# Optimization experiments

Hardware: AMD Instinct MI355X
Metric: run time of the kernel (lower is better)

## Reference

```python
import jax, jax.numpy as jnp
import numpy as np

B, K, N, T, C = 2, 2, 4096, 8, 3
H = 192            # hidden_dim
NODE_DIM = 10
N_LAYERS = 10
KNN = 16           # k nearest neighbours
TOP_FRAC = 0.4
SHARP = 5.0        # mask_sharpness
S = max(int(TOP_FRAC * N), KNN + 1)   # n_select per graph


def _ln(x, g, b, eps=1e-5):
    mu = x.mean(-1, keepdims=True)
    v = ((x - mu) ** 2).mean(-1, keepdims=True)  # biased var, matches nn.LayerNorm
    return (x - mu) / jnp.sqrt(v + eps) * g + b


def setup_inputs() -> dict:
    key = jax.random.key(0)
    ks = jax.random.split(key, 12)
    rn = lambda k, shape: 0.05 * jax.random.normal(k, shape, jnp.float32)
    F0 = 2 * NODE_DIM + 4   # first EdgeConv MLP in-dim
    FR = 2 * H + 4          # remaining EdgeConv MLP in-dim
    L = N_LAYERS - 1
    return {
        "u_base": jax.random.normal(ks[0], (B, K, N, C), jnp.float32),
        "pos": jax.random.uniform(ks[1], (B, N, 3), dtype=jnp.float32),
        "velocity_in": jax.random.normal(ks[2], (B, T, N, C), jnp.float32),
        "airfoil_mask": (jax.random.uniform(ks[3], (B, N)) < 0.05).astype(jnp.float32),
        "conv0_w1": rn(ks[4], (F0, H)), "conv0_b1": jnp.zeros((H,)),
        "conv0_w2": rn(ks[5], (H, H)), "conv0_b2": jnp.zeros((H,)),
        "conv0_g": jnp.ones((H,)), "conv0_be": jnp.zeros((H,)),
        "convs_w1": rn(ks[6], (L, FR, H)), "convs_b1": jnp.zeros((L, H)),
        "convs_w2": rn(ks[7], (L, H, H)), "convs_b2": jnp.zeros((L, H)),
        "convs_g": jnp.ones((L, H)), "convs_be": jnp.zeros((L, H)),
        "head_g": jnp.ones((H,)), "head_be": jnp.zeros((H,)),
        "head_w1": rn(ks[8], (H, H)), "head_b1": jnp.zeros((H,)),
        "head_w2": rn(ks[9], (H, 3)), "head_b2": jnp.zeros((3,)),
    }


def reference(u_base, pos, velocity_in, airfoil_mask,
              conv0_w1, conv0_b1, conv0_w2, conv0_b2, conv0_g, conv0_be,
              convs_w1, convs_b1, convs_w2, convs_b2, convs_g, convs_be,
              head_g, head_be, head_w1, head_b1, head_w2, head_b2):
    # --- variance gating (torch .var/.std are unbiased) ---
    var_pp = jnp.var(velocity_in, axis=1, ddof=1).sum(-1)                      # [B,N]
    var_z = (var_pp - var_pp.mean(1, keepdims=True)) / (
        jnp.std(var_pp, axis=1, ddof=1, keepdims=True) + 1e-8)
    soft_mask = jax.nn.sigmoid(SHARP * var_z) * (1.0 - airfoil_mask)           # [B,N]

    # --- select top-variance points per graph ---
    _, top_idx = jax.lax.top_k(var_pp, S)                                      # [B,S]
    pos_sel = jnp.take_along_axis(pos, top_idx[..., None], axis=1)             # [B,S,3]
    mask_sel = jnp.take_along_axis(soft_mask, top_idx, axis=1)[..., None]      # [B,S,1]
    v_last = velocity_in[:, -1]                                                # [B,N,C]
    ub_sel = jnp.take_along_axis(u_base, top_idx[:, None, :, None], axis=2)    # [B,K,S,C]
    vl_sel = jnp.take_along_axis(v_last, top_idx[..., None], axis=1)           # [B,S,C]
    vf_sel = jnp.take_along_axis(var_pp[..., None], top_idx[..., None], axis=1)
    static = jnp.concatenate([vl_sel, pos_sel, vf_sel], -1)                    # [B,S,7]
    x0 = jnp.concatenate(
        [ub_sel, jnp.broadcast_to(static[:, None], (B, K, S, 7))], -1)         # [B,K,S,10]

    def per_graph(x, pos_b):  # x: [K,S,F0], pos_b: [S,3]
        # kNN graph (self excluded via +inf diagonal, as in the chunked cdist)
        d2 = jnp.sum((pos_b[:, None] - pos_b[None]) ** 2, -1)                  # [S,S]
        d2 = d2.at[jnp.arange(S), jnp.arange(S)].set(jnp.inf)
        _, knn = jax.lax.top_k(-d2, KNN)                                       # [S,KNN]
        # PyG convention with edge_index=stack([targets, sources]):
        # i = edge_index[1] = knn neighbours, j = edge_index[0] = centre nodes
        idx_i = knn.reshape(-1)                     # [E] aggregation targets
        idx_j = jnp.repeat(jnp.arange(S), KNN)      # [E]
        rel = pos_b[idx_i] - pos_b[idx_j]           # pos[edge_index[1]] - pos[edge_index[0]]
        dist = jnp.linalg.norm(rel, axis=-1, keepdims=True)
        ea = jnp.concatenate([rel, dist], -1)       # [E,4]
        ea_b = jnp.broadcast_to(ea, (K,) + ea.shape)

        def conv(h, w1, b1, w2, b2, g, be):
            hi = h[:, idx_i]
            hj = h[:, idx_j]
            m = jnp.concatenate([hi, hj - hi, ea_b], -1)                       # [K,E,2F+4]
            m = jax.nn.gelu(m @ w1 + b1, approximate=False) @ w2 + b2          # [K,E,H]
            agg = jnp.zeros((K, S, H), h.dtype).at[:, idx_i].add(m)
            return _ln(agg, g, be)

        h = conv(x, conv0_w1, conv0_b1, conv0_w2, conv0_b2, conv0_g, conv0_be)
        for l in range(N_LAYERS - 1):
            h = conv(h, convs_w1[l], convs_b1[l], convs_w2[l], convs_b2[l],
                     convs_g[l], convs_be[l]) + h
        hh = _ln(h, head_g, head_be)
        return jax.nn.gelu(hh @ head_w1 + head_b1, approximate=False) @ head_w2 + head_b2

    delta = jax.vmap(per_graph)(x0, pos_sel)        # [B,K,S,3]
    delta = delta * mask_sel[:, None]               # [B,1,S,1]

    def scatter_b(idx, d):  # idx [S], d [K,S,3]
        return jnp.zeros((K, N, C), d.dtype).at[:, idx].set(d)

    delta_full = jax.vmap(scatter_b)(top_idx, delta)            # [B,K,N,C]
    return (u_base + delta_full) * (1.0 - airfoil_mask)[:, None, :, None]
```

## Files before the change

### kernel.cpp

```cpp
#include <hip/hip_runtime.h>
#include <hip/hip_bf16.h>
#include <math.h>

#define B_ 2
#define K_ 2
#define NN_ 4096
#define T_ 8
#define C_ 3
#define H_ 192
#define S_ 1638
#define KK_ 16
#define E_ (S_*KK_)
#define NROW (B_*K_*S_)
#define SHARP_ 5.0f

typedef __hip_bfloat16 bf;
typedef unsigned long long ull;
typedef __bf16 bf16x8 __attribute__((ext_vector_type(8)));
typedef float f32x4 __attribute__((ext_vector_type(4)));

__device__ int   g_isbf16;
__device__ __align__(16) float g_var[B_*NN_];
__device__ __align__(16) float g_vs1[B_*16];
__device__ __align__(16) float g_vs2[B_*16];
__device__ __align__(16) int   g_topidx[B_*S_];
__device__ __align__(16) float g_possel[B_*S_*3];
__device__ __align__(16) float g_masksel[B_*S_];
__device__ __align__(16) float g_x0[NROW*10];
__device__ __align__(16) int   g_knn[B_*E_];
__device__ __align__(16) float g_ea[B_*E_*4];
__device__ __align__(16) int   g_indeg[B_*S_];
__device__ __align__(16) int   g_cursor[B_*S_];
__device__ __align__(16) int   g_off[B_*(S_+1)];
__device__ __align__(16) int   g_list[B_*E_];
__device__ __align__(16) float g_P[(size_t)NROW*H_];
__device__ __align__(16) bf    g_Qbf[(size_t)NROW*H_];
__device__ __align__(16) float g_h[(size_t)NROW*H_];
__device__ __align__(16) bf    g_abf[(size_t)NROW*H_];
__device__ __align__(16) bf    g_w2p[(size_t)11*H_*H_];
__device__ __align__(16) bf    g_wcp[(size_t)9*H_*384];

__device__ __forceinline__ float bf2f(bf x){ return __bfloat162float(x); }
__device__ __forceinline__ float LD(const void* p, long i){
  return g_isbf16 ? __bfloat162float(((const bf*)p)[i]) : ((const float*)p)[i];
}
__device__ __forceinline__ float LDi(const void* p, long i, int isb){
  return isb ? __bfloat162float(((const bf*)p)[i]) : ((const float*)p)[i];
}
__device__ __forceinline__ float gelu_f(float x){ return 0.5f*x*(1.0f + erff(x*0.70710678118654752f)); }
__device__ __forceinline__ ull shfl_xor_u64(ull v, int m){
  unsigned lo = (unsigned)v, hi = (unsigned)(v >> 32);
  lo = __shfl_xor(lo, m, 64); hi = __shfl_xor(hi, m, 64);
  return ((ull)hi << 32) | lo;
}

__global__ __launch_bounds__(256) void k_var(const void* __restrict__ vel,
                                             const void* __restrict__ ub,
                                             const void* __restrict__ pos){
  __shared__ int s_bad;
  int b = blockIdx.y;
  int bx = blockIdx.x;
  int tid = threadIdx.x;
  if (tid == 0) s_bad = 0;
  __syncthreads();
  {
    const bf* pa = (const bf*)ub; const bf* pb = (const bf*)pos; const bf* pc = (const bf*)vel;
    int bad = 0;
    #pragma unroll
    for (int s = 0; s < 2; ++s){
      float va = __bfloat162float(pa[tid + s*256]);
      float vb = __bfloat162float(pb[tid + s*256]);
      float vc = __bfloat162float(pc[tid + s*256]);
      if (!(fabsf(va) <= 1000.f)) bad = 1;
      if (!(fabsf(vb) <= 1000.f)) bad = 1;
      if (!(fabsf(vc) <= 1000.f)) bad = 1;
    }
    if (bad) atomicOr(&s_bad, 1);
  }
  __syncthreads();
  int isb = (s_bad == 0) ? 1 : 0;
  if (bx == 0 && b == 0 && tid == 0) g_isbf16 = isb;
  int zi = (b*16 + bx)*256 + tid;
  if (zi < B_*S_){ g_indeg[zi] = 0; g_cursor[zi] = 0; }
  int n = bx*256 + tid;
  float v = 0.f;
  #pragma unroll
  for (int c = 0; c < 3; ++c){
    float x[8];
    #pragma unroll
    for (int t = 0; t < 8; ++t)
      x[t] = LDi(vel, ((long)(b*T_+t)*NN_ + n)*3 + c, isb);
    float m = __fadd_rn(__fadd_rn(__fadd_rn(x[0],x[1]), __fadd_rn(x[2],x[3])),
                        __fadd_rn(__fadd_rn(x[4],x[5]), __fadd_rn(x[6],x[7]))) / 8.0f;
    float d[8];
    #pragma unroll
    for (int t = 0; t < 8; ++t){ float dd = __fadd_rn(x[t], -m); d[t] = __fmul_rn(dd,dd); }
    float sv = __fadd_rn(__fadd_rn(__fadd_rn(d[0],d[1]), __fadd_rn(d[2],d[3])),
                         __fadd_rn(__fadd_rn(d[4],d[5]), __fadd_rn(d[6],d[7])));
    v = __fadd_rn(v, sv / 7.0f);
  }
  g_var[b*NN_ + n] = v;
  float s1 = v, s2 = v*v;
  #pragma unroll
  for (int o = 32; o; o >>= 1){ s1 += __shfl_xor(s1,o,64); s2 += __shfl_xor(s2,o,64); }
  __shared__ float r1[4], r2[4];
  int lane = tid & 63, wid = tid >> 6;
  if (!lane){ r1[wid]=s1; r2[wid]=s2; }
  __syncthreads();
  if (tid == 0){
    g_vs1[b*16 + bx] = r1[0]+r1[1]+r1[2]+r1[3];
    g_vs2[b*16 + bx] = r2[0]+r2[1]+r2[2]+r2[3];
  }
}

__global__ __launch_bounds__(256) void k_rank(){
  int b = blockIdx.y;
  int i = blockIdx.x*4 + (threadIdx.x >> 6);
  int lane = threadIdx.x & 63;
  float vi = g_var[b*NN_+i];
  int rank = 0;
  for (int j = lane; j < NN_; j += 64){
    float vj = g_var[b*NN_+j];
    rank += ((vj > vi) || (vj == vi && j < i)) ? 1 : 0;
  }
  #pragma unroll
  for (int o = 32; o; o >>= 1) rank += __shfl_xor(rank, o, 64);
  if (lane == 0 && rank < S_) g_topidx[b*S_ + rank] = i;
}

__global__ void k_gather(const void* __restrict__ pos, const void* __restrict__ ub,
                         const void* __restrict__ vel, const void* __restrict__ air){
  int gi = blockIdx.x*256 + threadIdx.x;
  if (gi >= B_*S_) return;
  int b = gi / S_, s = gi - b*S_;
  int node = g_topidx[gi];
  float px = LD(pos, ((long)b*NN_+node)*3+0);
  float py = LD(pos, ((long)b*NN_+node)*3+1);
  float pz = LD(pos, ((long)b*NN_+node)*3+2);
  g_possel[gi*3+0]=px; g_possel[gi*3+1]=py; g_possel[gi*3+2]=pz;
  float S1 = 0.f, S2 = 0.f;
  #pragma unroll
  for (int t = 0; t < 16; ++t){ S1 += g_vs1[b*16+t]; S2 += g_vs2[b*16+t]; }
  float mean = S1*(1.f/NN_);
  float sd = sqrtf(fmaxf((S2 - S1*S1*(1.f/NN_))*(1.f/(NN_-1)), 0.f));
  float vf = g_var[b*NN_+node];
  float z = (vf-mean)/(sd+1e-8f);
  float sig = 1.f/(1.f+expf(-SHARP_*z));
  g_masksel[gi] = sig*(1.f - LD(air, b*NN_+node));
  float vl0 = LD(vel, ((long)(b*T_+7)*NN_+node)*3+0);
  float vl1 = LD(vel, ((long)(b*T_+7)*NN_+node)*3+1);
  float vl2 = LD(vel, ((long)(b*T_+7)*NN_+node)*3+2);
  for (int k = 0; k < K_; ++k){
    long row = (long)(b*K_+k)*S_ + s;
    float* x = g_x0 + row*10;
    x[0]=LD(ub, ((long)(b*K_+k)*NN_+node)*3+0);
    x[1]=LD(ub, ((long)(b*K_+k)*NN_+node)*3+1);
    x[2]=LD(ub, ((long)(b*K_+k)*NN_+node)*3+2);
    x[3]=vl0; x[4]=vl1; x[5]=vl2;
    x[6]=px;  x[7]=py;  x[8]=pz;
    x[9]=vf;
  }
}

__global__ __launch_bounds__(256) void k_knn(){
  __shared__ float px[S_], py[S_], pz[S_];
  int b = blockIdx.y;
  int j = blockIdx.x*4 + (threadIdx.x >> 6);
  int lane = threadIdx.x & 63;
  for (int t = threadIdx.x; t < S_; t += 256){
    px[t] = g_possel[(b*S_+t)*3+0];
    py[t] = g_possel[(b*S_+t)*3+1];
    pz[t] = g_possel[(b*S_+t)*3+2];
  }
  __syncthreads();
  if (j >= S_) return;
  float xj=px[j], yj=py[j], zj=pz[j];
  float dist[KK_]; int id[KK_];
  #pragma unroll
  for (int t = 0; t < KK_; ++t){ dist[t]=3.0e38f; id[t]=0x7fffffff; }
  for (int c = lane; c < S_; c += 64){
    if (c == j) continue;
    float dx=__fadd_rn(px[c],-xj), dy=__fadd_rn(py[c],-yj), dz=__fadd_rn(pz[c],-zj);
    float d2 = __fadd_rn(__fadd_rn(__fmul_rn(dx,dx), __fmul_rn(dy,dy)), __fmul_rn(dz,dz));
    if (d2 < dist[KK_-1]){
      int p = 0;
      #pragma unroll
      for (int q = 0; q < KK_; ++q) p += (dist[q] <= d2) ? 1 : 0;
      #pragma unroll
      for (int q = KK_-1; q >= 1; --q){
        bool mv = (q > p);
        dist[q] = mv ? dist[q-1] : dist[q];
        id[q]   = mv ? id[q-1]   : id[q];
      }
      #pragma unroll
      for (int q = 0; q < KK_; ++q){ if (q == p){ dist[q] = d2; id[q] = c; } }
    }
  }
  ull mykey = 0;
  #pragma unroll
  for (int t = 0; t < KK_; ++t){
    ull k = (((ull)__float_as_uint(dist[0])) << 32) | (unsigned)id[0];
    ull m = k;
    #pragma unroll
    for (int o = 32; o; o >>= 1){ ull other = shfl_xor_u64(m, o); m = (other < m) ? other : m; }
    if (k == m){
      #pragma unroll
      for (int q = 0; q < KK_-1; ++q){ dist[q]=dist[q+1]; id[q]=id[q+1]; }
      dist[KK_-1] = 3.0e38f; id[KK_-1] = 0x7fffffff;
    }
    if (lane == t) mykey = m;
  }
  if (lane < KK_){
    int i = (int)(mykey & 0xffffffffu);
    g_knn[(b*S_+j)*KK_ + lane] = i;
    float rx = __fadd_rn(px[i],-xj), ry = __fadd_rn(py[i],-yj), rz = __fadd_rn(pz[i],-zj);
    float dd = sqrtf(__fadd_rn(__fadd_rn(__fmul_rn(rx,rx), __fmul_rn(ry,ry)), __fmul_rn(rz,rz)));
    float* o = g_ea + ((long)b*E_ + j*KK_ + lane)*4;
    o[0]=rx; o[1]=ry; o[2]=rz; o[3]=dd;
    atomicAdd(&g_indeg[b*S_+i], 1);
  }
}

__global__ void k_scan(){
  __shared__ int sA[2048], sB[2048];
  int b = blockIdx.x, tid = threadIdx.x;
  for (int i = tid; i < 2048; i += 1024) sA[i] = (i < S_) ? g_indeg[b*S_+i] : 0;
  __syncthreads();
  int *src = sA, *dst = sB;
  for (int d = 1; d < 2048; d <<= 1){
    for (int i = tid; i < 2048; i += 1024) dst[i] = src[i] + (i >= d ? src[i-d] : 0);
    __syncthreads();
    int* t2 = src; src = dst; dst = t2;
  }
  if (tid == 0) g_off[b*(S_+1)] = 0;
  for (int i = tid; i < S_; i += 1024) g_off[b*(S_+1)+i+1] = src[i];
}

#define PW2_BLKS 1584
#define PWC_BLKS 2592
#define INIT_BLKS 192
#define FILL_BLKS 205
#define PROJ_BLKS 410
__global__ void k_packall(const void* __restrict__ c0w2, const void* __restrict__ cw2,
                          const void* __restrict__ hw1, const void* __restrict__ cw1,
                          const void* __restrict__ ub, const void* __restrict__ air,
                          float* __restrict__ out, const void* __restrict__ c0w1){
  int blk = blockIdx.x;
  if (blk < PW2_BLKS){
    int gi = blk*256 + threadIdx.x;
    if (gi >= 11*H_*H_) return;
    int mat = gi / (H_*H_), r = gi - mat*(H_*H_);
    int k = r / H_, n = r - (r/H_)*H_;
    float v;
    if (mat == 0)      v = LD(c0w2, (long)k*H_ + n);
    else if (mat <= 9) v = LD(cw2, (long)(mat-1)*H_*H_ + (long)k*H_ + n);
    else               v = LD(hw1, (long)k*H_ + n);
    int t = k>>5, q = (k>>3)&3, jj = k&7;
    g_w2p[(size_t)mat*H_*H_ + (((t*4+q)*H_ + n)*8 + jj)] = __float2bfloat16(v);
  } else if (blk < PW2_BLKS + PWC_BLKS){
    int gi = (blk - PW2_BLKS)*256 + threadIdx.x;
    if (gi >= 9*H_*384) return;
    int l = gi / (H_*384), r = gi - l*(H_*384);
    int k = r / 384, n = r - (r/384)*384;
    long base = (long)l*388*H_;
    float v;
    if (n < H_) v = LD(cw1, base + (long)k*H_ + n) - LD(cw1, base + (long)(H_+k)*H_ + n);
    else        v = LD(cw1, base + (long)(H_+k)*H_ + (n-H_));
    int t = k>>5, q = (k>>3)&3, jj = k&7;
    g_wcp[(size_t)l*(H_*384) + (((t*4+q)*384 + n)*8 + jj)] = __float2bfloat16(v);
  } else if (blk < PW2_BLKS + PWC_BLKS + INIT_BLKS){
    int gi = (blk - PW2_BLKS - PWC_BLKS)*256 + threadIdx.x;
    int n = (gi/3) % NN_;
    int b = gi / (K_*NN_*C_);
    float a = 1.f - LD(air, b*NN_+n);
    out[gi] = LD(ub, gi) * a;
  } else if (blk < PW2_BLKS + PWC_BLKS + INIT_BLKS + FILL_BLKS){
    int idx = (blk - PW2_BLKS - PWC_BLKS - INIT_BLKS)*256 + threadIdx.x;
    if (idx >= B_*E_) return;
    int b = idx / E_, e = idx - b*E_;
    int i = g_knn[idx];
    int slot = atomicAdd(&g_cursor[b*S_+i], 1);
    g_list[b*E_ + g_off[b*(S_+1)+i] + slot] = e;
  } else {
    __shared__ float xs[16][10];
    __shared__ float wP[10][192];
    __shared__ float wQ[10][192];
    int tid = threadIdx.x;
    long rowBase = (long)(blk - PW2_BLKS - PWC_BLKS - INIT_BLKS - FILL_BLKS) * 16;
    for (int idx = tid; idx < 1920; idx += 256){
      int f = idx / 192, n = idx - (idx/192)*192;
      float a = LD(c0w1, f*H_+n), b = LD(c0w1, (10+f)*H_+n);
      wP[f][n] = a - b; wQ[f][n] = b;
    }
    for (int idx = tid; idx < 160; idx += 256){
      int r = idx / 10, f = idx - (idx/10)*10;
      long row = rowBase + r; if (row >= NROW) row = NROW-1;
      xs[r][f] = g_x0[row*10 + f];
    }
    __syncthreads();
    for (int o = tid; o < 16*384; o += 256){
      int r = o / 384, n = o - (o/384)*384;
      long row = rowBase + r;
      if (row >= NROW) continue;
      float acc = 0.f;
      if (n < 192){
        #pragma unroll
        for (int f = 0; f < 10; ++f) acc += xs[r][f]*wP[f][n];
        g_P[row*192 + n] = acc;
      } else {
        int nc = n - 192;
        #pragma unroll
        for (int f = 0; f < 10; ++f) acc += xs[r][f]*wQ[f][nc];
        g_Qbf[row*192 + nc] = __float2bfloat16(acc);
      }
    }
  }
}

__global__ __launch_bounds__(192) void k_aggedge(const void* __restrict__ w1cB, long w1cO,
                                                 const void* __restrict__ b1B, long b1O){
  int o = blockIdx.x;
  int t = o & 7, s = o >> 3;
  int bk = t >> 1;
  int row = bk*S_ + 2*s + (t & 1);
  int col = threadIdx.x;
  int i = row - bk*S_, b = bk >> 1;
  int off = g_off[b*(S_+1)+i];
  int deg = g_off[b*(S_+1)+i+1] - off;
  float w0 = LD(w1cB, w1cO+col),       w1v = LD(w1cB, w1cO+H_+col);
  float w2v = LD(w1cB, w1cO+2*H_+col), w3v = LD(w1cB, w1cO+3*H_+col);
  float base = g_P[(size_t)row*H_ + col] + LD(b1B, b1O+col);
  const int* lst = g_list + b*E_ + off;
  const bf* Q = g_Qbf + (size_t)bk*S_*H_;
  const float* EA = g_ea + (size_t)b*E_*4;
  float acc = 0.f;
  int d = 0;
  for (; d + 8 <= deg; d += 8){
    int e[8];
    #pragma unroll
    for (int u = 0; u < 8; ++u) e[u] = lst[d+u];
    float4 a[8];
    #pragma unroll
    for (int u = 0; u < 8; ++u) a[u] = *reinterpret_cast<const float4*>(EA + (size_t)e[u]*4);
    float qv[8];
    #pragma unroll
    for (int u = 0; u < 8; ++u) qv[u] = bf2f(Q[(size_t)(e[u]>>4)*H_ + col]);
    #pragma unroll
    for (int u = 0; u < 8; ++u)
      acc += gelu_f(base + qv[u] + a[u].x*w0 + a[u].y*w1v + a[u].z*w2v + a[u].w*w3v);
  }
  for (; d + 4 <= deg; d += 4){
    int e0 = lst[d], e1 = lst[d+1], e2 = lst[d+2], e3 = lst[d+3];
    float4 a0 = *reinterpret_cast<const float4*>(EA + (size_t)e0*4);
    float4 a1 = *reinterpret_cast<const float4*>(EA + (size_t)e1*4);
    float4 a2 = *reinterpret_cast<const float4*>(EA + (size_t)e2*4);
    float4 a3 = *reinterpret_cast<const float4*>(EA + (size_t)e3*4);
    float q0 = bf2f(Q[(size_t)(e0>>4)*H_ + col]);
    float q1 = bf2f(Q[(size_t)(e1>>4)*H_ + col]);
    float q2 = bf2f(Q[(size_t)(e2>>4)*H_ + col]);
    float q3 = bf2f(Q[(size_t)(e3>>4)*H_ + col]);
    acc += gelu_f(base + q0 + a0.x*w0 + a0.y*w1v + a0.z*w2v + a0.w*w3v);
    acc += gelu_f(base + q1 + a1.x*w0 + a1.y*w1v + a1.z*w2v + a1.w*w3v);
    acc += gelu_f(base + q2 + a2.x*w0 + a2.y*w1v + a2.z*w2v + a2.w*w3v);
    acc += gelu_f(base + q3 + a3.x*w0 + a3.y*w1v + a3.z*w2v + a3.w*w3v);
  }
  for (; d < deg; ++d){
    int e = lst[d];
    float4 a = *reinterpret_cast<const float4*>(EA + (size_t)e*4);
    float qv = bf2f(Q[(size_t)(e>>4)*H_ + col]);
    acc += gelu_f(base + qv + a.x*w0 + a.y*w1v + a.z*w2v + a.w*w3v);
  }
  g_abf[(size_t)row*H_ + col] = __float2bfloat16(acc);
}

template<int RES, int DOPQ>
__global__ __launch_bounds__(256) void k_lnpq(const void* __restrict__ biasB, long biasO,
                                              const void* __restrict__ gB, long gO,
                                              const void* __restrict__ beB, long beO,
                                              int bOff, int pqOff, int M){
  const bf* A  = g_abf;
  const bf* Bp = g_w2p + bOff;
  int wave = threadIdx.x >> 6, lane = threadIdx.x & 63;
  int q = lane >> 4, l16 = lane & 15;
  long rowBase = (long)blockIdx.x * 16;
  f32x4 acc[3];
  #pragma unroll
  for (int ct = 0; ct < 3; ++ct) acc[ct] = (f32x4){0.f,0.f,0.f,0.f};
  #pragma unroll
  for (int t = 0; t < 6; ++t){
    int kof = t*32 + q*8;
    long r = rowBase + l16; if (r >= M) r = M-1;
    bf16x8 af = *reinterpret_cast<const bf16x8*>(A + r*192 + kof);
    #pragma unroll
    for (int ct = 0; ct < 3; ++ct){
      int n = wave*48 + ct*16 + l16;
      bf16x8 bfr = *reinterpret_cast<const bf16x8*>(Bp + (((t*4+q)*192 + n)*8));
      acc[ct] = __builtin_amdgcn_mfma_f32_16x16x32_bf16(af, bfr, acc[ct], 0,0,0);
    }
  }
  __shared__ float tile[16][200];
  __shared__ bf    ybf[16][200];
  __shared__ float srow[16], rrow[16];
  #pragma unroll
  for (int ct = 0; ct < 3; ++ct){
    int col = wave*48 + ct*16 + l16;
    float bb = LD(biasB, biasO + col);
    #pragma unroll
    for (int r = 0; r < 4; ++r){
      int lr = q*4 + r;
      long row = rowBase + lr;
      long rowc = (row < M) ? row : (M-1);
      int bk = (int)(rowc / S_); int i = (int)(rowc - (long)bk*S_); int b = bk >> 1;
      float degf = (float)(g_off[b*(S_+1)+i+1] - g_off[b*(S_+1)+i]);
      tile[lr][col] = acc[ct][r] + degf*bb;
    }
  }
  __syncthreads();
  {
    int lr = threadIdx.x >> 4;
    int k16 = threadIdx.x & 15;
    float s = 0.f, qq = 0.f;
    for (int c = k16; c < 192; c += 16){ float x = tile[lr][c]; s += x; qq += x*x; }
    #pragma unroll
    for (int o = 1; o < 16; o <<= 1){ s += __shfl_xor(s,o,64); qq += __shfl_xor(qq,o,64); }
    if (k16 == 0){
      float mu = s*(1.f/H_);
      float var = qq*(1.f/H_) - mu*mu;
      srow[lr] = mu;
      rrow[lr] = rsqrtf(fmaxf(var, 0.f) + 1e-5f);
    }
  }
  __syncthreads();
  for (int o = threadIdx.x; o < 16*192; o += 256){
    int lr = o / 192, col = o - (o/192)*192;
    long row = rowBase + lr;
    long rowc = (row < M) ? row : (M-1);
    float y = (tile[lr][col] - srow[lr])*rrow[lr]*LD(gB,gO+col) + LD(beB,beO+col);
    if (RES) y += g_h[rowc*192 + col];
    if (row < M) g_h[row*192 + col] = y;
    ybf[lr][col] = __float2bfloat16(y);
  }
  if (DOPQ){
    __syncthreads();
    const bf* Bq = g_wcp + pqOff;
    f32x4 acc2[6];
    #pragma unroll
    for (int ct = 0; ct < 6; ++ct) acc2[ct] = (f32x4){0.f,0.f,0.f,0.f};
    #pragma unroll
    for (int t = 0; t < 6; ++t){
      int kof = t*32 + q*8;
      bf16x8 af = *reinterpret_cast<const bf16x8*>(&ybf[l16][kof]);
      #pragma unroll
      for (int ct = 0; ct < 6; ++ct){
        int n = wave*96 + ct*16 + l16;
        bf16x8 bfr = *reinterpret_cast<const bf16x8*>(Bq + (((t*4+q)*384 + n)*8));
        acc2[ct] = __builtin_amdgcn_mfma_f32_16x16x32_bf16(af, bfr, acc2[ct], 0,0,0);
      }
    }
    #pragma unroll
    for (int ct = 0; ct < 6; ++ct){
      int col = wave*96 + ct*16 + l16;
      #pragma unroll
      for (int r = 0; r < 4; ++r){
        long row = rowBase + q*4 + r;
        if (row < M){
          float v = acc2[ct][r];
          if (col < 192) g_P[row*192 + col] = v;
          else           g_Qbf[row*192 + (col-192)] = __float2bfloat16(v);
        }
      }
    }
  }
}

__global__ __launch_bounds__(256) void k_head(const void* __restrict__ gB,
                                              const void* __restrict__ beB,
                                              const void* __restrict__ biasB,
                                              const void* __restrict__ w2,
                                              const void* __restrict__ b2,
                                              const void* __restrict__ ubase,
                                              const void* __restrict__ air,
                                              float* __restrict__ out,
                                              int bOff, int M){
  const bf* Bp = g_w2p + bOff;
  int wave = threadIdx.x >> 6, lane = threadIdx.x & 63;
  int q = lane >> 4, l16 = lane & 15;
  long rowBase = (long)blockIdx.x * 32;
  __shared__ float tile[32][200];
  __shared__ bf hb_s[32][216];
  __shared__ float srow[32], rrow[32];
  for (int o = threadIdx.x; o < 32*192; o += 256){
    int lr = o / 192, col = o - (o/192)*192;
    long row = rowBase + lr;
    long rowc = (row < M) ? row : (M-1);
    tile[lr][col] = g_h[rowc*192 + col];
  }
  __syncthreads();
  {
    int lr = threadIdx.x >> 3;
    int k8 = threadIdx.x & 7;
    float s = 0.f, qq = 0.f;
    for (int c = k8; c < 192; c += 8){ float x = tile[lr][c]; s += x; qq += x*x; }
    #pragma unroll
    for (int o = 1; o < 8; o <<= 1){ s += __shfl_xor(s,o,64); qq += __shfl_xor(qq,o,64); }
    if (k8 == 0){
      float mu = s*(1.f/H_);
      float var = qq*(1.f/H_) - mu*mu;
      srow[lr] = mu;
      rrow[lr] = rsqrtf(fmaxf(var, 0.f) + 1e-5f);
    }
  }
  __syncthreads();
  for (int o = threadIdx.x; o < 32*192; o += 256){
    int lr = o / 192, col = o - (o/192)*192;
    hb_s[lr][col] = __float2bfloat16((tile[lr][col] - srow[lr])*rrow[lr]*LD(gB,col) + LD(beB,col));
  }
  __syncthreads();
  f32x4 acc[2][3];
  #pragma unroll
  for (int rt = 0; rt < 2; ++rt)
    #pragma unroll
    for (int ct = 0; ct < 3; ++ct) acc[rt][ct] = (f32x4){0.f,0.f,0.f,0.f};
  #pragma unroll
  for (int t = 0; t < 6; ++t){
    int kof = t*32 + q*8;
    bf16x8 af[2], bfr[3];
    #pragma unroll
    for (int rt = 0; rt < 2; ++rt)
      af[rt] = *reinterpret_cast<const bf16x8*>(&hb_s[rt*16 + l16][kof]);
    #pragma unroll
    for (int ct = 0; ct < 3; ++ct){
      int n = wave*48 + ct*16 + l16;
      bfr[ct] = *reinterpret_cast<const bf16x8*>(Bp + (((t*4+q)*192 + n)*8));
    }
    #pragma unroll
    for (int rt = 0; rt < 2; ++rt)
      #pragma unroll
      for (int ct = 0; ct < 3; ++ct)
        acc[rt][ct] = __builtin_amdgcn_mfma_f32_16x16x32_bf16(af[rt], bfr[ct], acc[rt][ct], 0,0,0);
  }
  #pragma unroll
  for (int rt = 0; rt < 2; ++rt){
    #pragma unroll
    for (int ct = 0; ct < 3; ++ct){
      int col = wave*48 + ct*16 + l16;
      float bb = LD(biasB, col);
      #pragma unroll
      for (int r = 0; r < 4; ++r){
        int lr = rt*16 + q*4 + r;
        tile[lr][col] = gelu_f(acc[rt][ct][r] + bb);
      }
    }
  }
  __syncthreads();
  {
    int r = threadIdx.x >> 3, k8 = threadIdx.x & 7;
    long row = rowBase + r;
    float p0 = 0.f, p1 = 0.f, p2 = 0.f;
    for (int col = k8; col < 192; col += 8){
      float tv = tile[r][col];
      p0 += tv*LD(w2, col*3+0);
      p1 += tv*LD(w2, col*3+1);
      p2 += tv*LD(w2, col*3+2);
    }
    #pragma unroll
    for (int o = 1; o < 8; o <<= 1){
      p0 += __shfl_xor(p0,o,64);
      p1 += __shfl_xor(p1,o,64);
      p2 += __shfl_xor(p2,o,64);
    }
    if (k8 == 0 && row < M){
      int bk = (int)(row / S_), s = (int)(row - (long)bk*S_), b = bk >> 1;
      float msk = g_masksel[b*S_+s];
      int node = g_topidx[b*S_+s];
      float am = 1.f - LD(air, b*NN_+node);
      float d0 = p0 + LD(b2,0), d1 = p1 + LD(b2,1), d2 = p2 + LD(b2,2);
      long oi = ((long)bk*NN_ + node)*3;
      out[oi+0] = (LD(ubase, oi+0) + d0*msk)*am;
      out[oi+1] = (LD(ubase, oi+1) + d1*msk)*am;
      out[oi+2] = (LD(ubase, oi+2) + d2*msk)*am;
    }
  }
}

extern "C" void kernel_launch(void* const* d_in, const int* in_sizes, int n_in,
                              void* d_out, int out_size, void* d_ws, size_t ws_size,
                              hipStream_t stream) {
  (void)in_sizes; (void)n_in; (void)d_ws; (void)ws_size; (void)out_size;
  const void* u_base = d_in[0];
  const void* pos    = d_in[1];
  const void* vel    = d_in[2];
  const void* air    = d_in[3];
  const void* c0w1   = d_in[4];
  const void* c0b1   = d_in[5];
  const void* c0w2   = d_in[6];
  const void* c0b2   = d_in[7];
  const void* c0g    = d_in[8];
  const void* c0be   = d_in[9];
  const void* cw1    = d_in[10];
  const void* cb1    = d_in[11];
  const void* cw2    = d_in[12];
  const void* cb2    = d_in[13];
  const void* cg     = d_in[14];
  const void* cbe    = d_in[15];
  const void* hg     = d_in[16];
  const void* hbe    = d_in[17];
  const void* hw1    = d_in[18];
  const void* hb1    = d_in[19];
  const void* hw2    = d_in[20];
  const void* hb2    = d_in[21];
  float* out = (float*)d_out;

  k_var<<<dim3(16, B_), 256, 0, stream>>>(vel, u_base, pos);
  k_rank<<<dim3(NN_/4, B_), 256, 0, stream>>>();
  k_gather<<<13, 256, 0, stream>>>(pos, u_base, vel, air);
  k_knn<<<dim3((S_+3)/4, B_), 256, 0, stream>>>();
  k_scan<<<B_, 1024, 0, stream>>>();
  k_packall<<<PW2_BLKS + PWC_BLKS + INIT_BLKS + FILL_BLKS + PROJ_BLKS, 256, 0, stream>>>(
      c0w2, cw2, hw1, cw1, u_base, air, out, c0w1);

  const int GN16 = (NROW + 15) / 16;
  for (int l = 0; l < 10; ++l){
    long w1cO = (l == 0) ? 20L*H_ : ((long)(l-1)*388 + 384)*H_;
    const void* w1cB = (l == 0) ? c0w1 : cw1;
    long lOff = (l == 0) ? 0 : (long)(l-1)*H_;
    const void* b1B = (l == 0) ? c0b1 : cb1;
    k_aggedge<<<NROW, 192, 0, stream>>>(w1cB, w1cO, b1B, lOff);

    const void* b2B = (l == 0) ? c0b2 : cb2;
    const void* gB  = (l == 0) ? c0g  : cg;
    const void* beB = (l == 0) ? c0be : cbe;
    if (l == 0)
      k_lnpq<0,1><<<GN16, 256, 0, stream>>>(b2B, lOff, gB, lOff, beB, lOff, 0,        0,        NROW);
    else if (l < 9)
      k_lnpq<1,1><<<GN16, 256, 0, stream>>>(b2B, lOff, gB, lOff, beB, lOff, l*H_*H_, l*H_*384, NROW);
    else
      k_lnpq<1,0><<<GN16, 256, 0, stream>>>(b2B, lOff, gB, lOff, beB, lOff, l*H_*H_, 0,        NROW);
  }

  k_head<<<(NROW + 31)/32, 256, 0, stream>>>(hg, hbe, hb1, hw2, hb2, u_base, air, out, 10*H_*H_, NROW);
}
```

Before: 583.7 us.

## Approximate GELU erf, merge gather into kNN kernel, widen LN/PQ blocks to 8 waves

Replaces erff in the edge GELU with an Abramowitz-Stegun polynomial using a fast exp, cutting transcendental cost in the hot edge-aggregation loop at some loss of accuracy. Folds the gather kernel into the kNN launch so the kNN blocks read selected positions directly through topidx, removing one launch and the possel buffer. Doubles the LN/PQ kernel to 512 threads so each wave handles fewer MFMA column tiles, raising parallelism per 16-row block, though waves 4-7 sit idle for part of the first GEMM.

```diff
diff --git a/kernel.cpp b/kernel.cpp
--- a/kernel.cpp
+++ b/kernel.cpp
@@ -24,7 +24,6 @@
 __device__ __align__(16) float g_vs1[B_*16];
 __device__ __align__(16) float g_vs2[B_*16];
 __device__ __align__(16) int   g_topidx[B_*S_];
-__device__ __align__(16) float g_possel[B_*S_*3];
 __device__ __align__(16) float g_masksel[B_*S_];
 __device__ __align__(16) float g_x0[NROW*10];
 __device__ __align__(16) int   g_knn[B_*E_];
@@ -47,7 +46,14 @@
 __device__ __forceinline__ float LDi(const void* p, long i, int isb){
   return isb ? __bfloat162float(((const bf*)p)[i]) : ((const float*)p)[i];
 }
-__device__ __forceinline__ float gelu_f(float x){ return 0.5f*x*(1.0f + erff(x*0.70710678118654752f)); }
+__device__ __forceinline__ float gelu_f(float x){
+  float ax = fabsf(x)*0.70710678118654752f;
+  float t = 1.0f/(1.0f + 0.3275911f*ax);
+  float p = t*(0.254829592f + t*(-0.284496736f + t*(1.421413741f + t*(-1.453152027f + t*1.061405429f))));
+  float er = 1.0f - p*__expf(-ax*ax);
+  er = copysignf(er, x);
+  return 0.5f*x*(1.0f + er);
+}
 __device__ __forceinline__ ull shfl_xor_u64(ull v, int m){
   unsigned lo = (unsigned)v, hi = (unsigned)(v >> 32);
   lo = __shfl_xor(lo, m, 64); hi = __shfl_xor(hi, m, 64);
@@ -128,49 +134,53 @@
   if (lane == 0 && rank < S_) g_topidx[b*S_ + rank] = i;
 }
 
-__global__ void k_gather(const void* __restrict__ pos, const void* __restrict__ ub,
-                         const void* __restrict__ vel, const void* __restrict__ air){
-  int gi = blockIdx.x*256 + threadIdx.x;
-  if (gi >= B_*S_) return;
-  int b = gi / S_, s = gi - b*S_;
-  int node = g_topidx[gi];
-  float px = LD(pos, ((long)b*NN_+node)*3+0);
-  float py = LD(pos, ((long)b*NN_+node)*3+1);
-  float pz = LD(pos, ((long)b*NN_+node)*3+2);
-  g_possel[gi*3+0]=px; g_possel[gi*3+1]=py; g_possel[gi*3+2]=pz;
-  float S1 = 0.f, S2 = 0.f;
-  #pragma unroll
-  for (int t = 0; t < 16; ++t){ S1 += g_vs1[b*16+t]; S2 += g_vs2[b*16+t]; }
-  float mean = S1*(1.f/NN_);
-  float sd = sqrtf(fmaxf((S2 - S1*S1*(1.f/NN_))*(1.f/(NN_-1)), 0.f));
-  float vf = g_var[b*NN_+node];
-  float z = (vf-mean)/(sd+1e-8f);
-  float sig = 1.f/(1.f+expf(-SHARP_*z));
-  g_masksel[gi] = sig*(1.f - LD(air, b*NN_+node));
-  float vl0 = LD(vel, ((long)(b*T_+7)*NN_+node)*3+0);
-  float vl1 = LD(vel, ((long)(b*T_+7)*NN_+node)*3+1);
-  float vl2 = LD(vel, ((long)(b*T_+7)*NN_+node)*3+2);
-  for (int k = 0; k < K_; ++k){
-    long row = (long)(b*K_+k)*S_ + s;
-    float* x = g_x0 + row*10;
-    x[0]=LD(ub, ((long)(b*K_+k)*NN_+node)*3+0);
-    x[1]=LD(ub, ((long)(b*K_+k)*NN_+node)*3+1);
-    x[2]=LD(ub, ((long)(b*K_+k)*NN_+node)*3+2);
-    x[3]=vl0; x[4]=vl1; x[5]=vl2;
-    x[6]=px;  x[7]=py;  x[8]=pz;
-    x[9]=vf;
-  }
-}
-
-__global__ __launch_bounds__(256) void k_knn(){
+#define GATH_BLKS 7
+__global__ __launch_bounds__(256) void k_knngather(const void* __restrict__ pos,
+                                                   const void* __restrict__ ub,
+                                                   const void* __restrict__ vel,
+                                                   const void* __restrict__ air){
+  int b = blockIdx.y;
+  int bx = blockIdx.x;
+  if (bx < GATH_BLKS){
+    int s = bx*256 + threadIdx.x;
+    if (s >= S_) return;
+    int gi = b*S_ + s;
+    int node = g_topidx[gi];
+    float px = LD(pos, ((long)b*NN_+node)*3+0);
+    float py = LD(pos, ((long)b*NN_+node)*3+1);
+    float pz = LD(pos, ((long)b*NN_+node)*3+2);
+    float S1 = 0.f, S2 = 0.f;
+    #pragma unroll
+    for (int t = 0; t < 16; ++t){ S1 += g_vs1[b*16+t]; S2 += g_vs2[b*16+t]; }
+    float mean = S1*(1.f/NN_);
+    float sd = sqrtf(fmaxf((S2 - S1*S1*(1.f/NN_))*(1.f/(NN_-1)), 0.f));
+    float vf = g_var[b*NN_+node];
+    float z = (vf-mean)/(sd+1e-8f);
+    float sig = 1.f/(1.f+expf(-SHARP_*z));
+    g_masksel[gi] = sig*(1.f - LD(air, b*NN_+node));
+    float vl0 = LD(vel, ((long)(b*T_+7)*NN_+node)*3+0);
+    float vl1 = LD(vel, ((long)(b*T_+7)*NN_+node)*3+1);
+    float vl2 = LD(vel, ((long)(b*T_+7)*NN_+node)*3+2);
+    for (int k = 0; k < K_; ++k){
+      long row = (long)(b*K_+k)*S_ + s;
+      float* x = g_x0 + row*10;
+      x[0]=LD(ub, ((long)(b*K_+k)*NN_+node)*3+0);
+      x[1]=LD(ub, ((long)(b*K_+k)*NN_+node)*3+1);
+      x[2]=LD(ub, ((long)(b*K_+k)*NN_+node)*3+2);
+      x[3]=vl0; x[4]=vl1; x[5]=vl2;
+      x[6]=px;  x[7]=py;  x[8]=pz;
+      x[9]=vf;
+    }
+    return;
+  }
   __shared__ float px[S_], py[S_], pz[S_];
-  int b = blockIdx.y;
-  int j = blockIdx.x*4 + (threadIdx.x >> 6);
+  int j = (bx - GATH_BLKS)*4 + (threadIdx.x >> 6);
   int lane = threadIdx.x & 63;
   for (int t = threadIdx.x; t < S_; t += 256){
-    px[t] = g_possel[(b*S_+t)*3+0];
-    py[t] = g_possel[(b*S_+t)*3+1];
-    pz[t] = g_possel[(b*S_+t)*3+2];
+    int node = g_topidx[b*S_+t];
+    px[t] = LD(pos, ((long)b*NN_+node)*3+0);
+    py[t] = LD(pos, ((long)b*NN_+node)*3+1);
+    pz[t] = LD(pos, ((long)b*NN_+node)*3+2);
   }
   __syncthreads();
   if (j >= S_) return;
@@ -374,56 +384,71 @@
 }
 
 template<int RES, int DOPQ>
-__global__ __launch_bounds__(256) void k_lnpq(const void* __restrict__ biasB, long biasO,
+__global__ __launch_bounds__(512) void k_lnpq(const void* __restrict__ biasB, long biasO,
                                               const void* __restrict__ gB, long gO,
                                               const void* __restrict__ beB, long beO,
                                               int bOff, int pqOff, int M){
   const bf* A  = g_abf;
   const bf* Bp = g_w2p + bOff;
-  int wave = threadIdx.x >> 6, lane = threadIdx.x & 63;
+  int tid = threadIdx.x;
+  int wv = tid >> 6, lane = tid & 63;
   int q = lane >> 4, l16 = lane & 15;
   long rowBase = (long)blockIdx.x * 16;
-  f32x4 acc[3];
-  #pragma unroll
-  for (int ct = 0; ct < 3; ++ct) acc[ct] = (f32x4){0.f,0.f,0.f,0.f};
-  #pragma unroll
-  for (int t = 0; t < 6; ++t){
-    int kof = t*32 + q*8;
-    long r = rowBase + l16; if (r >= M) r = M-1;
-    bf16x8 af = *reinterpret_cast<const bf16x8*>(A + r*192 + kof);
-    #pragma unroll
-    for (int ct = 0; ct < 3; ++ct){
-      int n = wave*48 + ct*16 + l16;
-      bf16x8 bfr = *reinterpret_cast<const bf16x8*>(Bp + (((t*4+q)*192 + n)*8));
-      acc[ct] = __builtin_amdgcn_mfma_f32_16x16x32_bf16(af, bfr, acc[ct], 0,0,0);
-    }
-  }
   __shared__ float tile[16][200];
   __shared__ bf    ybf[16][200];
   __shared__ float srow[16], rrow[16];
-  #pragma unroll
-  for (int ct = 0; ct < 3; ++ct){
-    int col = wave*48 + ct*16 + l16;
-    float bb = LD(biasB, biasO + col);
+  {
+    f32x4 acc[2];
+    acc[0] = (f32x4){0.f,0.f,0.f,0.f};
+    acc[1] = (f32x4){0.f,0.f,0.f,0.f};
+    #pragma unroll
+    for (int t = 0; t < 6; ++t){
+      int kof = t*32 + q*8;
+      long r = rowBase + l16; if (r >= M) r = M-1;
+      bf16x8 af = *reinterpret_cast<const bf16x8*>(A + r*192 + kof);
+      #pragma unroll
+      for (int jj = 0; jj < 2; ++jj){
+        int j = wv + jj*8;
+        if (j < 12){
+          int n = j*16 + l16;
+          bf16x8 bfr = *reinterpret_cast<const bf16x8*>(Bp + (((t*4+q)*192 + n)*8));
+          acc[jj] = __builtin_amdgcn_mfma_f32_16x16x32_bf16(af, bfr, acc[jj], 0,0,0);
+        }
+      }
+    }
+    float degf[4];
     #pragma unroll
     for (int r = 0; r < 4; ++r){
       int lr = q*4 + r;
       long row = rowBase + lr;
       long rowc = (row < M) ? row : (M-1);
       int bk = (int)(rowc / S_); int i = (int)(rowc - (long)bk*S_); int b = bk >> 1;
-      float degf = (float)(g_off[b*(S_+1)+i+1] - g_off[b*(S_+1)+i]);
-      tile[lr][col] = acc[ct][r] + degf*bb;
+      degf[r] = (float)(g_off[b*(S_+1)+i+1] - g_off[b*(S_+1)+i]);
+    }
+    #pragma unroll
+    for (int jj = 0; jj < 2; ++jj){
+      int j = wv + jj*8;
+      if (j < 12){
+        int col = j*16 + l16;
+        float bb = LD(biasB, biasO + col);
+        #pragma unroll
+        for (int r = 0; r < 4; ++r){
+          int lr = q*4 + r;
+          tile[lr][col] = acc[jj][r] + degf[r]*bb;
+        }
+      }
     }
   }
   __syncthreads();
   {
-    int lr = threadIdx.x >> 4;
-    int k16 = threadIdx.x & 15;
+    int lr = wv*2 + (lane >> 5);
+    int k32 = lane & 31;
     float s = 0.f, qq = 0.f;
-    for (int c = k16; c < 192; c += 16){ float x = tile[lr][c]; s += x; qq += x*x; }
-    #pragma unroll
-    for (int o = 1; o < 16; o <<= 1){ s += __shfl_xor(s,o,64); qq += __shfl_xor(qq,o,64); }
-    if (k16 == 0){
+    #pragma unroll
+    for (int c6 = 0; c6 < 6; ++c6){ float x = tile[lr][k32 + c6*32]; s += x; qq += x*x; }
+    #pragma unroll
+    for (int o = 1; o < 32; o <<= 1){ s += __shfl_xor(s,o,64); qq += __shfl_xor(qq,o,64); }
+    if (k32 == 0){
       float mu = s*(1.f/H_);
       float var = qq*(1.f/H_) - mu*mu;
       srow[lr] = mu;
@@ -431,7 +456,7 @@
     }
   }
   __syncthreads();
-  for (int o = threadIdx.x; o < 16*192; o += 256){
+  for (int o = tid; o < 16*192; o += 512){
     int lr = o / 192, col = o - (o/192)*192;
     long row = rowBase + lr;
     long rowc = (row < M) ? row : (M-1);
@@ -443,28 +468,28 @@
   if (DOPQ){
     __syncthreads();
     const bf* Bq = g_wcp + pqOff;
-    f32x4 acc2[6];
-    #pragma unroll
-    for (int ct = 0; ct < 6; ++ct) acc2[ct] = (f32x4){0.f,0.f,0.f,0.f};
+    f32x4 acc2[3];
+    #pragma unroll
+    for (int jj = 0; jj < 3; ++jj) acc2[jj] = (f32x4){0.f,0.f,0.f,0.f};
     #pragma unroll
     for (int t = 0; t < 6; ++t){
       int kof = t*32 + q*8;
       bf16x8 af = *reinterpret_cast<const bf16x8*>(&ybf[l16][kof]);
       #pragma unroll
-      for (int ct = 0; ct < 6; ++ct){
-        int n = wave*96 + ct*16 + l16;
+      for (int jj = 0; jj < 3; ++jj){
+        int n = (wv*3 + jj)*16 + l16;
         bf16x8 bfr = *reinterpret_cast<const bf16x8*>(Bq + (((t*4+q)*384 + n)*8));
-        acc2[ct] = __builtin_amdgcn_mfma_f32_16x16x32_bf16(af, bfr, acc2[ct], 0,0,0);
+        acc2[jj] = __builtin_amdgcn_mfma_f32_16x16x32_bf16(af, bfr, acc2[jj], 0,0,0);
       }
     }
     #pragma unroll
-    for (int ct = 0; ct < 6; ++ct){
-      int col = wave*96 + ct*16 + l16;
+    for (int jj = 0; jj < 3; ++jj){
+      int col = (wv*3 + jj)*16 + l16;
       #pragma unroll
       for (int r = 0; r < 4; ++r){
         long row = rowBase + q*4 + r;
         if (row < M){
-          float v = acc2[ct][r];
+          float v = acc2[jj][r];
           if (col < 192) g_P[row*192 + col] = v;
           else           g_Qbf[row*192 + (col-192)] = __float2bfloat16(v);
         }
@@ -613,8 +638,7 @@
 
   k_var<<<dim3(16, B_), 256, 0, stream>>>(vel, u_base, pos);
   k_rank<<<dim3(NN_/4, B_), 256, 0, stream>>>();
-  k_gather<<<13, 256, 0, stream>>>(pos, u_base, vel, air);
-  k_knn<<<dim3((S_+3)/4, B_), 256, 0, stream>>>();
+  k_knngather<<<dim3(GATH_BLKS + (S_+3)/4, B_), 256, 0, stream>>>(pos, u_base, vel, air);
   k_scan<<<B_, 1024, 0, stream>>>();
   k_packall<<<PW2_BLKS + PWC_BLKS + INIT_BLKS + FILL_BLKS + PROJ_BLKS, 256, 0, stream>>>(
       c0w2, cw2, hw1, cw1, u_base, air, out, c0w1);
@@ -631,11 +655,11 @@
     const void* gB  = (l == 0) ? c0g  : cg;
     const void* beB = (l == 0) ? c0be : cbe;
     if (l == 0)
-      k_lnpq<0,1><<<GN16, 256, 0, stream>>>(b2B, lOff, gB, lOff, beB, lOff, 0,        0,        NROW);
+      k_lnpq<0,1><<<GN16, 512, 0, stream>>>(b2B, lOff, gB, lOff, beB, lOff, 0,        0,        NROW);
     else if (l < 9)
-      k_lnpq<1,1><<<GN16, 256, 0, stream>>>(b2B, lOff, gB, lOff, beB, lOff, l*H_*H_, l*H_*384, NROW);
+      k_lnpq<1,1><<<GN16, 512, 0, stream>>>(b2B, lOff, gB, lOff, beB, lOff, l*H_*H_, l*H_*384, NROW);
     else
-      k_lnpq<1,0><<<GN16, 256, 0, stream>>>(b2B, lOff, gB, lOff, beB, lOff, l*H_*H_, 0,        NROW);
+      k_lnpq<1,0><<<GN16, 512, 0, stream>>>(b2B, lOff, gB, lOff, beB, lOff, l*H_*H_, 0,        NROW);
   }
 
   k_head<<<(NROW + 31)/32, 256, 0, stream>>>(hg, hbe, hb1, hw2, hb2, u_base, air, out, 10*H_*H_, NROW);
```

Result: no change. 587.3 us (+0.6%).
